# Optimization experiments

Hardware: AMD Instinct MI355X
Metric: run time of the kernel (lower is better)

The kernel has to match this reference:

```python
import jax, jax.numpy as jnp
import numpy as np

KMEANS_ITERS = 3   # soft-kmeans refinement iterations
TOPK = 12          # hardcoded in the torch module
EPS = 1e-8


def _gather(x, idx):
    # batched_index_select: x (b, c, m); idx (b, n, k) -> (b, c, n, k)
    return jax.vmap(lambda xb, ib: xb[:, ib])(x, idx)


def _soft_kmeans(points, cent):
    # points (b, n, c); cent (b, m, c) -> refined centroids and soft assignment weights (b, n, m)
    for _ in range(KMEANS_ITERS):
        p2 = jnp.sum(points * points, axis=-1)           # (b, n)
        c2 = jnp.sum(cent * cent, axis=-1)               # (b, m)
        logits = -(p2[:, :, None] - 2.0 * jnp.einsum('bnc,bmc->bnm', points, cent) + c2[:, None, :])
        w = jax.nn.softmax(logits, axis=-1)              # (b, n, m)
        cent = jnp.einsum('bnm,bnc->bmc', w, points) / (jnp.sum(w, axis=1)[:, :, None] + EPS)
    return cent, w


def setup_inputs():
    key = jax.random.key(0)
    k1, k2, k3 = jax.random.split(key, 3)
    b, c, H, W, k = 4, 192, 80, 80, 9
    n = H * W
    out_c = 192
    x = jax.random.normal(k1, (b, c, n, 1), dtype=jnp.float32)
    edge_index = jax.random.randint(k2, (2, b, n, k), 0, n)
    conv_w = jax.random.normal(k3, (out_c, 3 * c), dtype=jnp.float32) * (1.0 / np.sqrt(3 * c))
    conv_b = jnp.zeros((out_c,), dtype=jnp.float32)
    return {"x": x, "edge_index": edge_index, "conv_w": conv_w, "conv_b": conv_b,
            "num_centroids": 50, "H": 80, "W": 80}


def reference(x, edge_index, conv_w, conv_b, num_centroids, H, W):
    b, c, n, _ = x.shape
    xs = x[..., 0]                                        # (b, c, n)
    # initial centroids: adaptive_avg_pool2d to (5, 10); H, W chosen divisible so bins are uniform
    x_img = xs.reshape(b, c, H, W)
    init_cent = x_img.reshape(b, c, 5, H // 5, 10, W // 10).mean(axis=(3, 5)).reshape(b, c, 50)
    # edge gathers + max-relative reduction
    x_i = _gather(xs, edge_index[1])                      # (b, c, n, k)
    x_j = _gather(xs, edge_index[0])                      # (b, c, n, k)
    x_j = jnp.max(x_j - x_i, axis=-1, keepdims=True)      # (b, c, n, 1)
    # soft-kmeans centroid construction
    points = jnp.transpose(xs, (0, 2, 1))                 # (b, n, c)
    cent, weights = _soft_kmeans(points, jnp.transpose(init_cent, (0, 2, 1)))
    cent = jnp.transpose(cent, (0, 2, 1))                 # (b, c, m)
    # topk centroid routing + second gather-max stage
    _, nn_idx = jax.lax.top_k(weights, TOPK)              # (b, n, 12)
    x_jc = _gather(cent, nn_idx)                          # (b, c, n, 12)
    x_jc = jnp.max(x_jc - xs[..., None], axis=-1, keepdims=True)  # (b, c, n, 1)
    # channel-interleaved concat (matches torch stack on dim=2 then reshape to 3c)
    feat = jnp.stack([x, x_j, x_jc], axis=2).reshape(b, 3 * c, n)  # (b, 3c, n)
    # BasicConv: 1x1 conv + bias + relu (norm=None)
    out = jnp.einsum('oi,bin->bon', conv_w, feat) + conv_b[None, :, None]
    return jax.nn.relu(out)[..., None]                    # (b, out_c, n, 1)
```

## Files before the change

kernel.cpp:

```cpp
#include <hip/hip_runtime.h>
#include <hip/hip_bf16.h>
#include <math.h>

#define B_   4
#define C_   192
#define N_   6400
#define K_   9
#define M_   50
#define TK_  12
#define OC_  192
#define KC_  576
#define CH_  100
#define LSTR 53
#define TSTR 72
#define XSTR 40
#define GSTR 40
#define GPB  8

typedef __bf16 b16x8 __attribute__((ext_vector_type(8)));
typedef float f32x4 __attribute__((ext_vector_type(4)));

__device__ inline unsigned short f2b(float f) {
    union { __hip_bfloat16 h; unsigned short u; } v;
    v.h = __float2bfloat16(f);
    return v.u;
}
__device__ inline float b2f(unsigned short u) {
    union { float f; unsigned int i; } v;
    v.i = ((unsigned int)u) << 16;
    return v.f;
}
__device__ inline void up8(uint4 v, float* f) {
    unsigned int w[4] = {v.x, v.y, v.z, v.w};
#pragma unroll
    for (int i = 0; i < 4; i++) {
        f[2 * i]     = b2f((unsigned short)(w[i] & 0xffffu));
        f[2 * i + 1] = b2f((unsigned short)(w[i] >> 16));
    }
}
__device__ inline uint4 pack8(const float* f) {
    unsigned int w[4];
#pragma unroll
    for (int i = 0; i < 4; i++)
        w[i] = (unsigned int)f2b(f[2 * i]) | ((unsigned int)f2b(f[2 * i + 1]) << 16);
    uint4 v; v.x = w[0]; v.y = w[1]; v.z = w[2]; v.w = w[3];
    return v;
}

__global__ void k_transpose(const float* __restrict__ x, float* __restrict__ xt,
                            unsigned short* __restrict__ xt16,
                            unsigned short* __restrict__ xt16l,
                            const float* __restrict__ cw,
                            unsigned short* __restrict__ Wg16) {
    int tid = threadIdx.y * 32 + threadIdx.x;
    if (blockIdx.x >= 200) {
        int g = ((blockIdx.x - 200) * 24 + blockIdx.z * 6 + blockIdx.y) * 256 + tid;
        if (g < OC_ * KC_) {
            int r = g % KC_;
            Wg16[g] = f2b(cw[(g / KC_) * KC_ + (r % C_) * 3 + (r / C_)]);
        }
        return;
    }
    __shared__ float tile[32][33];
    int b = blockIdx.z;
    int p0 = blockIdx.x * 32, c0 = blockIdx.y * 32;
    int tx = threadIdx.x, ty = threadIdx.y;
    const float* xb = x + (size_t)b * C_ * N_;
    float* xtb = xt + (size_t)b * N_ * C_;
    unsigned short* xt16b = xt16 + (size_t)b * N_ * C_;
    unsigned short* xt16lb = xt16l + (size_t)b * N_ * C_;
#pragma unroll
    for (int i = 0; i < 4; i++) {
        int cc = ty + 8 * i;
        tile[cc][tx] = xb[(size_t)(c0 + cc) * N_ + p0 + tx];
    }
    __syncthreads();
#pragma unroll
    for (int i = 0; i < 4; i++) {
        int pp = ty + 8 * i;
        float v = tile[tx][pp];
        size_t o = (size_t)(p0 + pp) * C_ + c0 + tx;
        xtb[o] = v;
        unsigned short hi = f2b(v);
        xt16b[o] = hi;
        xt16lb[o] = f2b(v - b2f(hi));
    }
}

__global__ __launch_bounds__(192) void k_init_cent(const float* __restrict__ xt,
        float* __restrict__ cent, float* __restrict__ c2,
        unsigned short* __restrict__ centh, unsigned short* __restrict__ centl) {
    int m = blockIdx.x, b = blockIdx.y, c = threadIdx.x;
    if (m >= M_) {
        size_t o = ((size_t)b * 64 + m) * C_ + c;
        centh[o] = 0; centl[o] = 0;
        return;
    }
    int gy = m / 10, gx = m % 10;
    const float* xtb = xt + (size_t)b * N_ * C_;
    float s = 0.f;
    for (int yy = 0; yy < 16; yy++)
        for (int xx = 0; xx < 8; xx++) {
            int p = (gy * 16 + yy) * 80 + gx * 8 + xx;
            s += xtb[(size_t)p * C_ + c];
        }
    float v = s * (1.f / 128.f);
    cent[((size_t)b * M_ + m) * C_ + c] = v;
    size_t oh = ((size_t)b * 64 + m) * C_ + c;
    unsigned short hi = f2b(v);
    centh[oh] = hi;
    centl[oh] = f2b(v - b2f(hi));
    float q = v * v;
    __shared__ float red[3];
#pragma unroll
    for (int off = 32; off > 0; off >>= 1) q += __shfl_down(q, off, 64);
    if ((c & 63) == 0) red[c >> 6] = q;
    __syncthreads();
    if (c == 0) c2[(size_t)b * M_ + m] = red[0] + red[1] + red[2];
}

__global__ __launch_bounds__(512) void k_logits_upd(const float* __restrict__ xt,
        const unsigned short* __restrict__ xt16, const unsigned short* __restrict__ xt16l,
        const float* __restrict__ cent,
        const unsigned short* __restrict__ centh, const unsigned short* __restrict__ centl,
        const float* __restrict__ c2g,
        unsigned short* __restrict__ part, float* __restrict__ wsp,
        int* __restrict__ nn, int do_topk, int fast) {
    __shared__ alignas(16) char smem[51712];
    __shared__ float sred[512];
    float* Ac = (float*)smem;
    float* Bp = (float*)(smem + 4352);
    float* lg = (float*)(smem + 20480);
    unsigned short* lgTh = (unsigned short*)smem;
    unsigned short* lgTl = (unsigned short*)(smem + 9216);
    unsigned short* xTh = (unsigned short*)(smem + 18432);
    unsigned short* xTl = (unsigned short*)(smem + 35072);
    int b = blockIdx.y;
    int blk = blockIdx.x;
    int p0 = blk * 64;
    int tid = threadIdx.x;
    int tx = tid & 15, ty = (tid >> 4) & 15;
    int lr = (tid >> 2) & 63, lq = tid & 3;
    int wave = tid >> 6, lane = tid & 63;
    int m16 = lane & 15, q = lane >> 4;
    const float* xb = xt + ((size_t)b * N_ + p0) * C_;
    const unsigned short* x16b = xt16 + ((size_t)b * N_ + p0) * C_;
    const unsigned short* x16lb = xt16l + ((size_t)b * N_ + p0) * C_;
    if (fast) {
        const unsigned short* chg = centh + (size_t)b * 64 * C_;
        const unsigned short* clg = centl + (size_t)b * 64 * C_;
        int pg = wave & 3, mh = wave >> 2;
        f32x4 acc1[2];
#pragma unroll
        for (int i = 0; i < 2; i++) acc1[i] = (f32x4){0.f, 0.f, 0.f, 0.f};
#pragma unroll
        for (int kt = 0; kt < 6; kt++) {
            int kg = kt * 32;
            size_t xo = (size_t)(pg * 16 + m16) * C_ + kg + q * 8;
            b16x8 bh = *(const b16x8*)&x16b[xo];
            b16x8 bl = *(const b16x8*)&x16lb[xo];
#pragma unroll
            for (int t = 0; t < 2; t++) {
                int mt = mh * 2 + t;
                size_t co = (size_t)(mt * 16 + m16) * C_ + kg + q * 8;
                b16x8 ah = *(const b16x8*)&chg[co];
                b16x8 al = *(const b16x8*)&clg[co];
                acc1[t] = __builtin_amdgcn_mfma_f32_16x16x32_bf16(ah, bh, acc1[t], 0, 0, 0);
                acc1[t] = __builtin_amdgcn_mfma_f32_16x16x32_bf16(ah, bl, acc1[t], 0, 0, 0);
                acc1[t] = __builtin_amdgcn_mfma_f32_16x16x32_bf16(al, bh, acc1[t], 0, 0, 0);
            }
        }
#pragma unroll
        for (int t = 0; t < 2; t++) {
#pragma unroll
            for (int r = 0; r < 4; r++) {
                int m = (mh * 2 + t) * 16 + q * 4 + r;
                if (m < M_) {
                    float c2v = c2g[(size_t)b * M_ + m];
                    lg[(pg * 16 + m16) * LSTR + m] = 2.f * acc1[t][r] - c2v;
                }
            }
        }
    } else {
        const float* cb = cent + (size_t)b * M_ * C_;
        float acc[4][4];
#pragma unroll
        for (int i = 0; i < 4; i++)
#pragma unroll
            for (int j = 0; j < 4; j++) acc[i][j] = 0.f;
        for (int kt = 0; kt < 12; kt++) {
            int kg = kt * 16;
            float4 cv = make_float4(0.f, 0.f, 0.f, 0.f);
            float4 pv = make_float4(0.f, 0.f, 0.f, 0.f);
            if (tid < 256) {
                if (lr < M_) cv = *(const float4*)&cb[(size_t)lr * C_ + kg + 4 * lq];
                pv = *(const float4*)&xb[(size_t)lr * C_ + kg + 4 * lq];
            }
            __syncthreads();
            if (tid < 256) {
                Ac[(4 * lq + 0) * 68 + lr] = cv.x; Ac[(4 * lq + 1) * 68 + lr] = cv.y;
                Ac[(4 * lq + 2) * 68 + lr] = cv.z; Ac[(4 * lq + 3) * 68 + lr] = cv.w;
                Bp[(4 * lq + 0) * 68 + lr] = pv.x; Bp[(4 * lq + 1) * 68 + lr] = pv.y;
                Bp[(4 * lq + 2) * 68 + lr] = pv.z; Bp[(4 * lq + 3) * 68 + lr] = pv.w;
            }
            __syncthreads();
            if (tid < 256) {
#pragma unroll
                for (int kk = 0; kk < 16; kk++) {
                    float4 a = *(const float4*)&Ac[kk * 68 + 4 * ty];
                    float4 bb = *(const float4*)&Bp[kk * 68 + 4 * tx];
                    acc[0][0] += a.x * bb.x; acc[0][1] += a.x * bb.y; acc[0][2] += a.x * bb.z; acc[0][3] += a.x * bb.w;
                    acc[1][0] += a.y * bb.x; acc[1][1] += a.y * bb.y; acc[1][2] += a.y * bb.z; acc[1][3] += a.y * bb.w;
                    acc[2][0] += a.z * bb.x; acc[2][1] += a.z * bb.y; acc[2][2] += a.z * bb.z; acc[2][3] += a.z * bb.w;
                    acc[3][0] += a.w * bb.x; acc[3][1] += a.w * bb.y; acc[3][2] += a.w * bb.z; acc[3][3] += a.w * bb.w;
                }
            }
        }
        __syncthreads();
        if (tid < 256) {
#pragma unroll
            for (int i = 0; i < 4; i++) {
                int m = 4 * ty + i;
                if (m < M_) {
                    float c2v = c2g[(size_t)b * M_ + m];
#pragma unroll
                    for (int j = 0; j < 4; j++)
                        lg[(4 * tx + j) * LSTR + m] = 2.f * acc[i][j] - c2v;
                }
            }
        }
    }
    __syncthreads();
    {
        int p = tid & 63, prt = tid >> 6;
        int m0 = prt * 7;
        int m1 = (m0 + 7 > M_) ? M_ : m0 + 7;
        float* row = &lg[p * LSTR];
        float mx = -1e30f;
        for (int m = m0; m < m1; m++) mx = fmaxf(mx, row[m]);
        sred[prt * 64 + p] = mx;
        __syncthreads();
        mx = -1e30f;
#pragma unroll
        for (int k = 0; k < 8; k++) mx = fmaxf(mx, sred[k * 64 + p]);
        float s = 0.f;
        for (int m = m0; m < m1; m++) {
            float e = expf(row[m] - mx);
            row[m] = e;
            s += e;
        }
        __syncthreads();
        sred[prt * 64 + p] = s;
        __syncthreads();
        s = 0.f;
#pragma unroll
        for (int k = 0; k < 8; k++) s += sred[k * 64 + p];
        float inv = 1.f / s;
        for (int m = m0; m < m1; m++) row[m] *= inv;
    }
    __syncthreads();
    for (int j = tid; j < 64 * 64; j += 512) {
        int m = j >> 6, p = j & 63;
        float w = (m < M_) ? lg[p * LSTR + m] : 0.f;
        unsigned short hi = f2b(w);
        lgTh[m * TSTR + p] = hi;
        lgTl[m * TSTR + p] = f2b(w - b2f(hi));
    }
    __syncthreads();
    if (do_topk && tid < 64) {
        float* row = &lg[tid * LSTR];
        int* nb = nn + ((size_t)b * N_ + p0 + tid) * TK_;
        for (int r = 0; r < TK_; r++) {
            float bv = -1.f;
            int bi = 0;
            for (int m = 0; m < M_; m++) {
                float v = row[m];
                if (v > bv) { bv = v; bi = m; }
            }
            nb[r] = bi;
            row[bi] = -1.f;
        }
    }
    int mt2 = wave >> 1, cbase = (wave & 1) * 7;
    f32x4 acc2[7];
#pragma unroll
    for (int i = 0; i < 7; i++) acc2[i] = (f32x4){0.f, 0.f, 0.f, 0.f};
    for (int h = 0; h < 2; h++) {
        __syncthreads();
        for (int j = tid; j < 32 * 24; j += 512) {
            int pl = j & 31, ko = (j >> 5) * 8;
            int4 vh = *(const int4*)&x16b[(size_t)(h * 32 + pl) * C_ + ko];
            int4 vl = *(const int4*)&x16lb[(size_t)(h * 32 + pl) * C_ + ko];
            const unsigned short* ph = (const unsigned short*)&vh;
            const unsigned short* pv = (const unsigned short*)&vl;
#pragma unroll
            for (int i = 0; i < 8; i++) {
                xTh[(ko + i) * XSTR + pl] = ph[i];
                xTl[(ko + i) * XSTR + pl] = pv[i];
            }
        }
        for (int j = tid; j < 32 * 16; j += 512) {
            int pl = j & 31, c = C_ + (j >> 5);
            xTh[c * XSTR + pl] = (c == C_) ? f2b(1.f) : 0;
            xTl[c * XSTR + pl] = 0;
        }
        __syncthreads();
        b16x8 ah = *(const b16x8*)&lgTh[(mt2 * 16 + m16) * TSTR + h * 32 + q * 8];
        b16x8 al = *(const b16x8*)&lgTl[(mt2 * 16 + m16) * TSTR + h * 32 + q * 8];
#pragma unroll
        for (int ci = 0; ci < 7; ci++) {
            int ct = cbase + ci;
            if (ct >= 13) continue;
            b16x8 bh = *(const b16x8*)&xTh[(ct * 16 + m16) * XSTR + q * 8];
            b16x8 bl = *(const b16x8*)&xTl[(ct * 16 + m16) * XSTR + q * 8];
            acc2[ci] = __builtin_amdgcn_mfma_f32_16x16x32_bf16(ah, bh, acc2[ci], 0, 0, 0);
            acc2[ci] = __builtin_amdgcn_mfma_f32_16x16x32_bf16(ah, bl, acc2[ci], 0, 0, 0);
            acc2[ci] = __builtin_amdgcn_mfma_f32_16x16x32_bf16(al, bh, acc2[ci], 0, 0, 0);
        }
    }
    unsigned short* pb = part + ((size_t)b * CH_ + blk) * (size_t)(M_ * C_);
    int mbase = mt2 * 16 + q * 4;
#pragma unroll
    for (int ci = 0; ci < 7; ci++) {
        int ct = cbase + ci;
        if (ct >= 13) continue;
        int c = ct * 16 + m16;
#pragma unroll
        for (int r = 0; r < 4; r++) {
            int mm = mbase + r;
            if (mm >= M_) continue;
            float v = acc2[ci][r];
            if (c < C_) pb[(size_t)mm * C_ + c] = f2b(v);
            else if (c == C_) wsp[((size_t)b * CH_ + blk) * M_ + mm] = v;
        }
    }
}

__global__ __launch_bounds__(768) void k_upd_reduce(const unsigned short* __restrict__ part,
        const float* __restrict__ wsp, float* __restrict__ cent, float* __restrict__ c2,
        unsigned short* __restrict__ cent16,
        unsigned short* __restrict__ centh, unsigned short* __restrict__ centl, int last) {
    int m = blockIdx.x, b = blockIdx.y;
    int tid = threadIdx.x;
    int c = tid % 192, g = tid / 192;
    __shared__ float pred[3][192];
    __shared__ float sws;
    __shared__ float red[3];
    const unsigned short* pp = part + (((size_t)b * CH_ + (size_t)g * 25) * M_ + m) * (size_t)C_ + c;
    float s = 0.f;
    for (int ch = 0; ch < 25; ch++)
        s += b2f(pp[(size_t)ch * M_ * C_]);
    if (g) pred[g - 1][c] = s;
    if (tid < 64) {
        float w = wsp[((size_t)b * CH_ + tid) * M_ + m];
        if (tid + 64 < CH_) w += wsp[((size_t)b * CH_ + tid + 64) * M_ + m];
#pragma unroll
        for (int off = 32; off > 0; off >>= 1) w += __shfl_down(w, off, 64);
        if (tid == 0) sws = w + 1e-8f;
    }
    __syncthreads();
    if (g == 0) {
        float v = (s + pred[0][c] + pred[1][c] + pred[2][c]) / sws;
        size_t o = ((size_t)b * M_ + m) * C_ + c;
        cent[o] = v;
        if (last) cent16[o] = f2b(v);
        size_t oh = ((size_t)b * 64 + m) * C_ + c;
        unsigned short hi = f2b(v);
        centh[oh] = hi;
        centl[oh] = f2b(v - b2f(hi));
        float q = v * v;
#pragma unroll
        for (int off = 32; off > 0; off >>= 1) q += __shfl_down(q, off, 64);
        if ((c & 63) == 0) red[c >> 6] = q;
    }
    __syncthreads();
    if (tid == 0) c2[(size_t)b * M_ + m] = red[0] + red[1] + red[2];
}

__global__ __launch_bounds__(192) void k_gather(const unsigned short* __restrict__ xt16,
        const unsigned short* __restrict__ cent16, const int* __restrict__ edge,
        const int* __restrict__ nn, unsigned short* __restrict__ xjt16,
        unsigned short* __restrict__ xjct16) {
    __shared__ int sidx[GPB * (2 * K_ + TK_)];
    int b = blockIdx.y;
    int p0 = blockIdx.x * GPB;
    int tid = threadIdx.x;
    for (int j = tid; j < GPB * (2 * K_ + TK_); j += 192) {
        int g = j / (2 * K_ + TK_), r = j % (2 * K_ + TK_);
        size_t base = (size_t)b * N_ + p0 + g;
        int v;
        if (r < K_) v = edge[base * K_ + r];
        else if (r < 2 * K_) v = edge[(size_t)B_ * N_ * K_ + base * K_ + (r - K_)];
        else v = nn[base * TK_ + (r - 2 * K_)];
        sidx[j] = v;
    }
    __syncthreads();
    int g = tid / 24, t = tid % 24;
    int ch0 = t * 8;
    int p = p0 + g;
    const unsigned short* xb = xt16 + (size_t)b * N_ * C_;
    const unsigned short* cb = cent16 + (size_t)b * M_ * C_;
    const int* si = &sidx[g * (2 * K_ + TK_)];
    float xv[8], ta[8], tb[8], mj[8], mc[8];
    up8(*(const uint4*)&xb[(size_t)p * C_ + ch0], xv);
#pragma unroll
    for (int e = 0; e < 8; e++) { mj[e] = -1e30f; mc[e] = -1e30f; }
#pragma unroll
    for (int kk = 0; kk < K_; kk++) {
        up8(*(const uint4*)&xb[(size_t)si[kk] * C_ + ch0], ta);
        up8(*(const uint4*)&xb[(size_t)si[K_ + kk] * C_ + ch0], tb);
#pragma unroll
        for (int e = 0; e < 8; e++) mj[e] = fmaxf(mj[e], ta[e] - tb[e]);
    }
#pragma unroll
    for (int kk = 0; kk < TK_; kk++) {
        up8(*(const uint4*)&cb[(size_t)si[2 * K_ + kk] * C_ + ch0], ta);
#pragma unroll
        for (int e = 0; e < 8; e++) mc[e] = fmaxf(mc[e], ta[e]);
    }
#pragma unroll
    for (int e = 0; e < 8; e++) mc[e] -= xv[e];
    size_t o = ((size_t)b * N_ + p) * C_ + ch0;
    *(uint4*)&xjt16[o] = pack8(mj);
    *(uint4*)&xjct16[o] = pack8(mc);
}

__global__ __launch_bounds__(256) void k_gemm(const unsigned short* __restrict__ Wg16,
        const unsigned short* __restrict__ xt16, const unsigned short* __restrict__ xjt16,
        const unsigned short* __restrict__ xjct16, const float* __restrict__ bias,
        float* __restrict__ out) {
    __shared__ short As[192 * GSTR];
    __shared__ short Bs[64 * GSTR];
    int b = blockIdx.y;
    int po = blockIdx.x * 64;
    int tid = threadIdx.x;
    int wave = tid >> 6, lane = tid & 63;
    int m16 = lane & 15, q = lane >> 4;
    const unsigned short* s0 = xt16 + (size_t)b * N_ * C_;
    const unsigned short* s1 = xjt16 + (size_t)b * N_ * C_;
    const unsigned short* s2 = xjct16 + (size_t)b * N_ * C_;
    f32x4 acc[12];
#pragma unroll
    for (int i = 0; i < 12; i++) acc[i] = (f32x4){0.f, 0.f, 0.f, 0.f};
    int brow = tid >> 2, bch = tid & 3;
    for (int kt = 0; kt < 18; kt++) {
        int kg = kt * 32;
        int prt = kg / C_, koff = kg - prt * C_;
        const unsigned short* src = (prt == 0) ? s0 : ((prt == 1) ? s1 : s2);
        int4 av[3];
#pragma unroll
        for (int t = 0; t < 3; t++) {
            int idx = t * 256 + tid;
            av[t] = *(const int4*)&Wg16[(size_t)(idx >> 2) * KC_ + kg + (idx & 3) * 8];
        }
        int4 bv = *(const int4*)&src[(size_t)(po + brow) * C_ + koff + bch * 8];
        __syncthreads();
#pragma unroll
        for (int t = 0; t < 3; t++) {
            int idx = t * 256 + tid;
            *(int4*)&As[(idx >> 2) * GSTR + (idx & 3) * 8] = av[t];
        }
        *(int4*)&Bs[brow * GSTR + bch * 8] = bv;
        __syncthreads();
        b16x8 bf = *(const b16x8*)&Bs[(wave * 16 + m16) * GSTR + q * 8];
#pragma unroll
        for (int of = 0; of < 12; of++) {
            b16x8 af = *(const b16x8*)&As[(of * 16 + m16) * GSTR + q * 8];
            acc[of] = __builtin_amdgcn_mfma_f32_16x16x32_bf16(af, bf, acc[of], 0, 0, 0);
        }
    }
    int p = po + wave * 16 + m16;
#pragma unroll
    for (int of = 0; of < 12; of++) {
        int o = of * 16 + q * 4;
        float4 bv = *(const float4*)&bias[o];
        float bia[4] = {bv.x, bv.y, bv.z, bv.w};
#pragma unroll
        for (int r = 0; r < 4; r++)
            out[((size_t)b * OC_ + o + r) * N_ + p] = fmaxf(acc[of][r] + bia[r], 0.f);
    }
}

extern "C" void kernel_launch(void* const* d_in, const int* in_sizes, int n_in,
                              void* d_out, int out_size, void* d_ws, size_t ws_size,
                              hipStream_t stream) {
    (void)in_sizes; (void)n_in; (void)out_size; (void)ws_size;
    const float* x   = (const float*)d_in[0];
    const int* edge  = (const int*)d_in[1];
    const float* cw  = (const float*)d_in[2];
    const float* cbi = (const float*)d_in[3];
    float* ws = (float*)d_ws;
    size_t o = 0;
    float* xt   = ws + o; o += (size_t)B_ * N_ * C_;
    unsigned short* xt16 = (unsigned short*)(ws + o); o += (size_t)B_ * N_ * C_ / 2;
    unsigned short* xt16l = (unsigned short*)(ws + o); o += (size_t)B_ * N_ * C_ / 2;
    unsigned short* Wg16 = (unsigned short*)(ws + o); o += (size_t)OC_ * KC_ / 2;
    float* cent = ws + o; o += (size_t)B_ * M_ * C_;
    unsigned short* cent16 = (unsigned short*)(ws + o); o += (size_t)B_ * M_ * C_ / 2;
    unsigned short* centh = (unsigned short*)(ws + o); o += (size_t)B_ * 64 * C_ / 2;
    unsigned short* centl = (unsigned short*)(ws + o); o += (size_t)B_ * 64 * C_ / 2;
    float* c2   = ws + o; o += (size_t)B_ * M_;
    unsigned short* part = (unsigned short*)(ws + o); o += (size_t)B_ * CH_ * M_ * C_ / 2;
    float* wsp  = ws + o; o += (size_t)B_ * CH_ * M_;
    int* nn = (int*)(ws + o); o += (size_t)B_ * N_ * TK_;
    unsigned short* xjt16  = (unsigned short*)(ws + o); o += (size_t)B_ * N_ * C_ / 2;
    unsigned short* xjct16 = (unsigned short*)(ws + o); o += (size_t)B_ * N_ * C_ / 2;
    float* outp = (float*)d_out;

    k_transpose<<<dim3(218, C_ / 32, B_), dim3(32, 8), 0, stream>>>(x, xt, xt16, xt16l, cw, Wg16);
    k_init_cent<<<dim3(64, B_), dim3(192), 0, stream>>>(xt, cent, c2, centh, centl);
    for (int it = 0; it < 3; it++) {
        k_logits_upd<<<dim3(CH_, B_), dim3(512), 0, stream>>>(xt, xt16, xt16l, cent,
            centh, centl, c2, part, wsp, nn, (it == 2) ? 1 : 0, (it < 2) ? 1 : 0);
        k_upd_reduce<<<dim3(M_, B_), dim3(768), 0, stream>>>(part, wsp, cent, c2,
            cent16, centh, centl, (it == 2) ? 1 : 0);
    }
    k_gather<<<dim3(N_ / GPB, B_), dim3(192), 0, stream>>>(xt16, cent16, edge, nn, xjt16, xjct16);
    k_gemm<<<dim3(N_ / 64, B_), dim3(256), 0, stream>>>(Wg16, xt16, xjt16, xjct16, cbi, outp);
}
```

Baseline: 246.5 us.

## Fuse edge/centroid gather-max into the 1x1 conv GEMM and split-K slow logits

Moves the gather-max stage into the GEMM kernel, building the x_j and x_jc features per 64-point tile in shared memory instead of writing and re-reading two full bf16 intermediates through global memory, and drops one launch. Also splits the K loop of the fp32 logits path across both 256-thread halves of the block and reduces the partial results through shared memory. The fused kernel uses 64KB of LDS and fewer threads per point for the gather, which can reduce occupancy and latency hiding.

```diff
diff --git a/kernel.cpp b/kernel.cpp
--- a/kernel.cpp
+++ b/kernel.cpp
@@ -15,7 +15,7 @@
 #define TSTR 72
 #define XSTR 40
 #define GSTR 40
-#define GPB  8
+#define FSTR 392
 
 typedef __bf16 b16x8 __attribute__((ext_vector_type(8)));
 typedef float f32x4 __attribute__((ext_vector_type(4)));
@@ -128,8 +128,6 @@
         int* __restrict__ nn, int do_topk, int fast) {
     __shared__ alignas(16) char smem[51712];
     __shared__ float sred[512];
-    float* Ac = (float*)smem;
-    float* Bp = (float*)(smem + 4352);
     float* lg = (float*)(smem + 20480);
     unsigned short* lgTh = (unsigned short*)smem;
     unsigned short* lgTl = (unsigned short*)(smem + 9216);
@@ -139,8 +137,6 @@
     int blk = blockIdx.x;
     int p0 = blk * 64;
     int tid = threadIdx.x;
-    int tx = tid & 15, ty = (tid >> 4) & 15;
-    int lr = (tid >> 2) & 63, lq = tid & 3;
     int wave = tid >> 6, lane = tid & 63;
     int m16 = lane & 15, q = lane >> 4;
     const float* xb = xt + ((size_t)b * N_ + p0) * C_;
@@ -183,49 +179,57 @@
         }
     } else {
         const float* cb = cent + (size_t)b * M_ * C_;
+        int grp = tid >> 8;
+        int ltid = tid & 255;
+        int ltx = ltid & 15, lty = ltid >> 4;
+        int llr = ltid >> 2, llq = ltid & 3;
+        float* Acg = (float*)(smem + grp * 8704);
+        float* Bpg = (float*)(smem + grp * 8704 + 4352);
         float acc[4][4];
 #pragma unroll
         for (int i = 0; i < 4; i++)
 #pragma unroll
             for (int j = 0; j < 4; j++) acc[i][j] = 0.f;
-        for (int kt = 0; kt < 12; kt++) {
-            int kg = kt * 16;
+        for (int kt = 0; kt < 6; kt++) {
+            int kg = (grp * 6 + kt) * 16;
             float4 cv = make_float4(0.f, 0.f, 0.f, 0.f);
-            float4 pv = make_float4(0.f, 0.f, 0.f, 0.f);
-            if (tid < 256) {
-                if (lr < M_) cv = *(const float4*)&cb[(size_t)lr * C_ + kg + 4 * lq];
-                pv = *(const float4*)&xb[(size_t)lr * C_ + kg + 4 * lq];
-            }
+            if (llr < M_) cv = *(const float4*)&cb[(size_t)llr * C_ + kg + 4 * llq];
+            float4 pv = *(const float4*)&xb[(size_t)llr * C_ + kg + 4 * llq];
             __syncthreads();
-            if (tid < 256) {
-                Ac[(4 * lq + 0) * 68 + lr] = cv.x; Ac[(4 * lq + 1) * 68 + lr] = cv.y;
-                Ac[(4 * lq + 2) * 68 + lr] = cv.z; Ac[(4 * lq + 3) * 68 + lr] = cv.w;
-                Bp[(4 * lq + 0) * 68 + lr] = pv.x; Bp[(4 * lq + 1) * 68 + lr] = pv.y;
-                Bp[(4 * lq + 2) * 68 + lr] = pv.z; Bp[(4 * lq + 3) * 68 + lr] = pv.w;
-            }
+            Acg[(4 * llq + 0) * 68 + llr] = cv.x; Acg[(4 * llq + 1) * 68 + llr] = cv.y;
+            Acg[(4 * llq + 2) * 68 + llr] = cv.z; Acg[(4 * llq + 3) * 68 + llr] = cv.w;
+            Bpg[(4 * llq + 0) * 68 + llr] = pv.x; Bpg[(4 * llq + 1) * 68 + llr] = pv.y;
+            Bpg[(4 * llq + 2) * 68 + llr] = pv.z; Bpg[(4 * llq + 3) * 68 + llr] = pv.w;
             __syncthreads();
-            if (tid < 256) {
-#pragma unroll
-                for (int kk = 0; kk < 16; kk++) {
-                    float4 a = *(const float4*)&Ac[kk * 68 + 4 * ty];
-                    float4 bb = *(const float4*)&Bp[kk * 68 + 4 * tx];
-                    acc[0][0] += a.x * bb.x; acc[0][1] += a.x * bb.y; acc[0][2] += a.x * bb.z; acc[0][3] += a.x * bb.w;
-                    acc[1][0] += a.y * bb.x; acc[1][1] += a.y * bb.y; acc[1][2] += a.y * bb.z; acc[1][3] += a.y * bb.w;
-                    acc[2][0] += a.z * bb.x; acc[2][1] += a.z * bb.y; acc[2][2] += a.z * bb.z; acc[2][3] += a.z * bb.w;
-                    acc[3][0] += a.w * bb.x; acc[3][1] += a.w * bb.y; acc[3][2] += a.w * bb.z; acc[3][3] += a.w * bb.w;
-                }
-            }
-        }
-        __syncthreads();
-        if (tid < 256) {
+#pragma unroll
+            for (int kk = 0; kk < 16; kk++) {
+                float4 a = *(const float4*)&Acg[kk * 68 + 4 * lty];
+                float4 bb = *(const float4*)&Bpg[kk * 68 + 4 * ltx];
+                acc[0][0] += a.x * bb.x; acc[0][1] += a.x * bb.y; acc[0][2] += a.x * bb.z; acc[0][3] += a.x * bb.w;
+                acc[1][0] += a.y * bb.x; acc[1][1] += a.y * bb.y; acc[1][2] += a.y * bb.z; acc[1][3] += a.y * bb.w;
+                acc[2][0] += a.z * bb.x; acc[2][1] += a.z * bb.y; acc[2][2] += a.z * bb.z; acc[2][3] += a.z * bb.w;
+                acc[3][0] += a.w * bb.x; acc[3][1] += a.w * bb.y; acc[3][2] += a.w * bb.z; acc[3][3] += a.w * bb.w;
+            }
+        }
+        float* scr = (float*)(smem + 35072);
+        if (grp == 1) {
+#pragma unroll
+            for (int i = 0; i < 4; i++)
+#pragma unroll
+                for (int j = 0; j < 4; j++) scr[ltid * 16 + i * 4 + j] = acc[i][j];
+        }
+        __syncthreads();
+        if (grp == 0) {
 #pragma unroll
             for (int i = 0; i < 4; i++) {
-                int m = 4 * ty + i;
+                int m = 4 * lty + i;
                 if (m < M_) {
                     float c2v = c2g[(size_t)b * M_ + m];
 #pragma unroll
-                    for (int j = 0; j < 4; j++)
-                        lg[(4 * tx + j) * LSTR + m] = 2.f * acc[i][j] - c2v;
+                    for (int j = 0; j < 4; j++) {
+                        float t = acc[i][j] + scr[ltid * 16 + i * 4 + j];
+                        lg[(4 * ltx + j) * LSTR + m] = 2.f * t - c2v;
+                    }
                 }
             }
         }
@@ -377,17 +381,24 @@
     if (tid == 0) c2[(size_t)b * M_ + m] = red[0] + red[1] + red[2];
 }
 
-__global__ __launch_bounds__(192) void k_gather(const unsigned short* __restrict__ xt16,
-        const unsigned short* __restrict__ cent16, const int* __restrict__ edge,
-        const int* __restrict__ nn, unsigned short* __restrict__ xjt16,
-        unsigned short* __restrict__ xjct16) {
-    __shared__ int sidx[GPB * (2 * K_ + TK_)];
+__global__ __launch_bounds__(256) void k_gemm(const unsigned short* __restrict__ Wg16,
+        const unsigned short* __restrict__ xt16, const unsigned short* __restrict__ cent16,
+        const int* __restrict__ edge, const int* __restrict__ nn,
+        const float* __restrict__ bias, float* __restrict__ out) {
+    __shared__ alignas(16) char smem[65536];
+    unsigned short* feat = (unsigned short*)smem;
+    int* sidx = (int*)(smem + 50176);
+    short* As = (short*)(smem + 50176);
     int b = blockIdx.y;
-    int p0 = blockIdx.x * GPB;
+    int po = blockIdx.x * 64;
     int tid = threadIdx.x;
-    for (int j = tid; j < GPB * (2 * K_ + TK_); j += 192) {
-        int g = j / (2 * K_ + TK_), r = j % (2 * K_ + TK_);
-        size_t base = (size_t)b * N_ + p0 + g;
+    int wave = tid >> 6, lane = tid & 63;
+    int m16 = lane & 15, q = lane >> 4;
+    const unsigned short* xb = xt16 + (size_t)b * N_ * C_;
+    const unsigned short* cb = cent16 + (size_t)b * M_ * C_;
+    for (int j = tid; j < 64 * 30; j += 256) {
+        int g = j / 30, r = j % 30;
+        size_t base = (size_t)b * N_ + po + g;
         int v;
         if (r < K_) v = edge[base * K_ + r];
         else if (r < 2 * K_) v = edge[(size_t)B_ * N_ * K_ + base * K_ + (r - K_)];
@@ -395,74 +406,58 @@
         sidx[j] = v;
     }
     __syncthreads();
-    int g = tid / 24, t = tid % 24;
-    int ch0 = t * 8;
-    int p = p0 + g;
-    const unsigned short* xb = xt16 + (size_t)b * N_ * C_;
-    const unsigned short* cb = cent16 + (size_t)b * M_ * C_;
-    const int* si = &sidx[g * (2 * K_ + TK_)];
-    float xv[8], ta[8], tb[8], mj[8], mc[8];
-    up8(*(const uint4*)&xb[(size_t)p * C_ + ch0], xv);
-#pragma unroll
-    for (int e = 0; e < 8; e++) { mj[e] = -1e30f; mc[e] = -1e30f; }
-#pragma unroll
-    for (int kk = 0; kk < K_; kk++) {
-        up8(*(const uint4*)&xb[(size_t)si[kk] * C_ + ch0], ta);
-        up8(*(const uint4*)&xb[(size_t)si[K_ + kk] * C_ + ch0], tb);
-#pragma unroll
-        for (int e = 0; e < 8; e++) mj[e] = fmaxf(mj[e], ta[e] - tb[e]);
-    }
-#pragma unroll
-    for (int kk = 0; kk < TK_; kk++) {
-        up8(*(const uint4*)&cb[(size_t)si[2 * K_ + kk] * C_ + ch0], ta);
-#pragma unroll
-        for (int e = 0; e < 8; e++) mc[e] = fmaxf(mc[e], ta[e]);
-    }
-#pragma unroll
-    for (int e = 0; e < 8; e++) mc[e] -= xv[e];
-    size_t o = ((size_t)b * N_ + p) * C_ + ch0;
-    *(uint4*)&xjt16[o] = pack8(mj);
-    *(uint4*)&xjct16[o] = pack8(mc);
-}
-
-__global__ __launch_bounds__(256) void k_gemm(const unsigned short* __restrict__ Wg16,
-        const unsigned short* __restrict__ xt16, const unsigned short* __restrict__ xjt16,
-        const unsigned short* __restrict__ xjct16, const float* __restrict__ bias,
-        float* __restrict__ out) {
-    __shared__ short As[192 * GSTR];
-    __shared__ short Bs[64 * GSTR];
-    int b = blockIdx.y;
-    int po = blockIdx.x * 64;
-    int tid = threadIdx.x;
-    int wave = tid >> 6, lane = tid & 63;
-    int m16 = lane & 15, q = lane >> 4;
-    const unsigned short* s0 = xt16 + (size_t)b * N_ * C_;
-    const unsigned short* s1 = xjt16 + (size_t)b * N_ * C_;
-    const unsigned short* s2 = xjct16 + (size_t)b * N_ * C_;
+    {
+        int g = tid >> 2, t = tid & 3;
+        const int* si = &sidx[g * 30];
+        int p = po + g;
+        for (int cc = 0; cc < 6; cc++) {
+            int ch0 = t * 48 + cc * 8;
+            float xv[8], ta[8], tb[8], mj[8], mc[8];
+            up8(*(const uint4*)&xb[(size_t)p * C_ + ch0], xv);
+#pragma unroll
+            for (int e = 0; e < 8; e++) { mj[e] = -1e30f; mc[e] = -1e30f; }
+#pragma unroll
+            for (int kk = 0; kk < K_; kk++) {
+                up8(*(const uint4*)&xb[(size_t)si[kk] * C_ + ch0], ta);
+                up8(*(const uint4*)&xb[(size_t)si[K_ + kk] * C_ + ch0], tb);
+#pragma unroll
+                for (int e = 0; e < 8; e++) mj[e] = fmaxf(mj[e], ta[e] - tb[e]);
+            }
+#pragma unroll
+            for (int kk = 0; kk < TK_; kk++) {
+                up8(*(const uint4*)&cb[(size_t)si[2 * K_ + kk] * C_ + ch0], ta);
+#pragma unroll
+                for (int e = 0; e < 8; e++) mc[e] = fmaxf(mc[e], ta[e]);
+            }
+#pragma unroll
+            for (int e = 0; e < 8; e++) mc[e] -= xv[e];
+            *(uint4*)&feat[(size_t)g * FSTR + ch0] = pack8(mj);
+            *(uint4*)&feat[(size_t)g * FSTR + 192 + ch0] = pack8(mc);
+        }
+    }
     f32x4 acc[12];
 #pragma unroll
     for (int i = 0; i < 12; i++) acc[i] = (f32x4){0.f, 0.f, 0.f, 0.f};
-    int brow = tid >> 2, bch = tid & 3;
     for (int kt = 0; kt < 18; kt++) {
         int kg = kt * 32;
-        int prt = kg / C_, koff = kg - prt * C_;
-        const unsigned short* src = (prt == 0) ? s0 : ((prt == 1) ? s1 : s2);
         int4 av[3];
 #pragma unroll
         for (int t = 0; t < 3; t++) {
             int idx = t * 256 + tid;
             av[t] = *(const int4*)&Wg16[(size_t)(idx >> 2) * KC_ + kg + (idx & 3) * 8];
         }
-        int4 bv = *(const int4*)&src[(size_t)(po + brow) * C_ + koff + bch * 8];
         __syncthreads();
 #pragma unroll
         for (int t = 0; t < 3; t++) {
             int idx = t * 256 + tid;
             *(int4*)&As[(idx >> 2) * GSTR + (idx & 3) * 8] = av[t];
         }
-        *(int4*)&Bs[brow * GSTR + bch * 8] = bv;
-        __syncthreads();
-        b16x8 bf = *(const b16x8*)&Bs[(wave * 16 + m16) * GSTR + q * 8];
+        __syncthreads();
+        b16x8 bf;
+        if (kt < 6)
+            bf = *(const b16x8*)&xb[(size_t)(po + wave * 16 + m16) * C_ + kg + q * 8];
+        else
+            bf = *(const b16x8*)&feat[(size_t)(wave * 16 + m16) * FSTR + (kg - C_) + q * 8];
 #pragma unroll
         for (int of = 0; of < 12; of++) {
             b16x8 af = *(const b16x8*)&As[(of * 16 + m16) * GSTR + q * 8];
@@ -503,8 +498,6 @@
     unsigned short* part = (unsigned short*)(ws + o); o += (size_t)B_ * CH_ * M_ * C_ / 2;
     float* wsp  = ws + o; o += (size_t)B_ * CH_ * M_;
     int* nn = (int*)(ws + o); o += (size_t)B_ * N_ * TK_;
-    unsigned short* xjt16  = (unsigned short*)(ws + o); o += (size_t)B_ * N_ * C_ / 2;
-    unsigned short* xjct16 = (unsigned short*)(ws + o); o += (size_t)B_ * N_ * C_ / 2;
     float* outp = (float*)d_out;
 
     k_transpose<<<dim3(218, C_ / 32, B_), dim3(32, 8), 0, stream>>>(x, xt, xt16, xt16l, cw, Wg16);
@@ -515,6 +508,5 @@
         k_upd_reduce<<<dim3(M_, B_), dim3(768), 0, stream>>>(part, wsp, cent, c2,
             cent16, centh, centl, (it == 2) ? 1 : 0);
     }
-    k_gather<<<dim3(N_ / GPB, B_), dim3(192), 0, stream>>>(xt16, cent16, edge, nn, xjt16, xjct16);
-    k_gemm<<<dim3(N_ / 64, B_), dim3(256), 0, stream>>>(Wg16, xt16, xjt16, xjct16, cbi, outp);
-}
+    k_gemm<<<dim3(N_ / 64, B_), dim3(256), 0, stream>>>(Wg16, xt16, cent16, edge, nn, cbi, outp);
+}
```

Result: slower. 308.2 us (+25.0%).
